# Optimization experiments

Hardware: AMD Instinct MI355X
Metric: run time of the kernel (lower is better)

Reference implementation:

```python
import jax, jax.numpy as jnp
import numpy as np

B, N, D, H = 8, 2048, 128, 4
DH = D // H
EPS_LN = 1e-5


def setup_inputs() -> dict:
    key = jax.random.key(0)
    ks = jax.random.split(key, 9)
    x = jax.random.normal(ks[0], (B, N, D), dtype=jnp.float32)
    u = jax.random.uniform(ks[1], (N, N), dtype=jnp.float32)
    adj = jnp.where(u > 0.5, u, 0.0)
    adj = adj.at[jnp.arange(N), jnp.arange(N)].set(1.0)
    W = jax.random.normal(ks[2], (D, D), dtype=jnp.float32) * (1.0 / np.sqrt(D))
    a_src = jax.random.normal(ks[3], (H, DH), dtype=jnp.float32) * 0.02
    a_dst = jax.random.normal(ks[4], (H, DH), dtype=jnp.float32) * 0.02
    Wo = jax.random.normal(ks[5], (D, D), dtype=jnp.float32) * (1.0 / np.sqrt(D))
    bo = jnp.zeros((D,), dtype=jnp.float32)
    gamma = jnp.ones((D,), dtype=jnp.float32)
    beta = jnp.zeros((D,), dtype=jnp.float32)
    return {"x": x, "adj_static": adj, "W": W, "a_src": a_src, "a_dst": a_dst,
            "Wo": Wo, "bo": bo, "gamma": gamma, "beta": beta}


def reference(x, adj_static, W, a_src, a_dst, Wo, bo, gamma, beta):
    # h: (B, H, N, DH)
    h = (x @ W.T).reshape(B, N, H, DH).transpose(0, 2, 1, 3)
    src = jnp.einsum('bhnd,hd->bhn', h, a_src)  # (B, H, N)
    dst = jnp.einsum('bhnd,hd->bhn', h, a_dst)  # (B, H, N)
    e = jax.nn.leaky_relu(src[..., :, None] + dst[..., None, :], 0.2)  # (B,H,N,N)
    logA = jnp.log(jnp.clip(adj_static, 1e-8))[None, None]
    mask = (adj_static > 0)[None, None]
    e = jnp.where(mask, e + logA, -jnp.inf)
    attn = jax.nn.softmax(e, axis=-1)  # dropout is identity in eval mode
    out = attn @ h  # (B, H, N, DH)
    out = out.transpose(0, 2, 1, 3).reshape(B, N, D)
    out = out @ Wo.T + bo
    y = x + out
    mu = jnp.mean(y, axis=-1, keepdims=True)
    var = jnp.mean(jnp.square(y - mu), axis=-1, keepdims=True)
    return (y - mu) * jax.lax.rsqrt(var + EPS_LN) * gamma + beta
```

## Files before the change

kernel.cpp:

```cpp
#include <hip/hip_runtime.h>

typedef short bf16x8 __attribute__((ext_vector_type(8)));
typedef _Float16 f16x8 __attribute__((ext_vector_type(8)));
typedef float f32x4  __attribute__((ext_vector_type(4)));
typedef float f32x2  __attribute__((ext_vector_type(2)));
typedef int   i32x4  __attribute__((ext_vector_type(4)));
typedef unsigned int u32x2 __attribute__((ext_vector_type(2)));

#define DEV static __device__ __forceinline__
#define LOG2E 1.4426950408889634f

DEV float bfu_to_f(unsigned short s) { return __builtin_bit_cast(float, (unsigned int)s << 16); }
DEV unsigned short f_to_bf(float f) {
  unsigned int u = __builtin_bit_cast(unsigned int, f);
  u += 0x7fffu + ((u >> 16) & 1u);
  return (unsigned short)(u >> 16);
}
DEV unsigned int pack_bf_rne(float lo, float hi) {
  return (unsigned int)f_to_bf(lo) | ((unsigned int)f_to_bf(hi) << 16);
}
DEV unsigned int pk_f16(float a, float b) {
  auto h = __builtin_amdgcn_cvt_pkrtz(a, b);
  return __builtin_bit_cast(unsigned int, h);
}
DEV unsigned short f_to_f16(float a) { return __builtin_bit_cast(unsigned short, (_Float16)a); }
DEV float nexp2(float x) {
#if __has_builtin(__builtin_amdgcn_exp2f)
  return __builtin_amdgcn_exp2f(x);
#else
  return exp2f(x);
#endif
}

DEV bool detect_f32(const void* adj) { return ((const float*)adj)[0] == 1.0f; }

template<bool F32> DEV float ldS(const void* p, size_t i) {
  if constexpr (F32) return ((const float*)p)[i];
  else               return bfu_to_f(((const unsigned short*)p)[i]);
}
template<bool F32> DEV void ld8f(const void* p, size_t i, float* o) {
  if constexpr (F32) {
    const float* f = (const float*)p + i;
    f32x4 a = *(const f32x4*)f, b = *(const f32x4*)(f + 4);
    o[0]=a[0]; o[1]=a[1]; o[2]=a[2]; o[3]=a[3];
    o[4]=b[0]; o[5]=b[1]; o[6]=b[2]; o[7]=b[3];
  } else {
    i32x4 w = *(const i32x4*)((const unsigned short*)p + i);
#pragma unroll
    for (int k = 0; k < 4; ++k) {
      unsigned int u = (unsigned int)w[k];
      o[2*k]   = __builtin_bit_cast(float, u << 16);
      o[2*k+1] = __builtin_bit_cast(float, u & 0xffff0000u);
    }
  }
}
template<bool F32> DEV bf16x8 ldfrag(const void* p, size_t i) {
  if constexpr (F32) {
    float o[8]; ld8f<true>(p, i, o);
    union { bf16x8 v; unsigned short u[8]; } r;
#pragma unroll
    for (int k = 0; k < 8; ++k) r.u[k] = f_to_bf(o[k]);
    return r.v;
  } else {
    return __builtin_bit_cast(bf16x8, *(const i32x4*)((const unsigned short*)p + i));
  }
}


__global__ __launch_bounds__(256) void k_prep(const void* __restrict__ adj,
                                              unsigned short* __restrict__ adjS) {
  const int tid = threadIdx.x, lane = tid & 63, w = tid >> 6;
  const int T = blockIdx.x * 4 + w;
  const int it = T >> 6, jt = T & 63;
  const int m = lane & 15, q = lane >> 4;
  const size_t src = (size_t)(it * 16 + m) * 2048 + jt * 32 + q * 8;
  float f[8];
  if (detect_f32(adj)) ld8f<true>(adj, src, f);
  else                 ld8f<false>(adj, src, f);
  i32x4 o;
#pragma unroll
  for (int k = 0; k < 4; ++k) o[k] = (int)pk_f16(f[2*k], f[2*k+1]);
  *(i32x4*)(adjS + (size_t)T * 512 + lane * 8) = o;
}

template<bool F32> DEV void k_h_body(const void* __restrict__ x, const void* __restrict__ W,
                                     unsigned short* __restrict__ vtS,
                                     unsigned short (&t_s)[16][136]) {
  const int tid = threadIdx.x, lane = tid & 63, wave = tid >> 6;
  const int nt = blockIdx.x >> 3, ct = blockIdx.x & 7;
  const int m = lane & 15, q = lane >> 4;
  bf16x8 wf[4];
#pragma unroll
  for (int k = 0; k < 4; ++k)
    wf[k] = ldfrag<F32>(W, (size_t)(ct * 16 + m) * 128 + q * 8 + k * 32);
#pragma unroll
  for (int s = 0; s < 2; ++s) {
    const int nsub = wave * 2 + s;
    const size_t xr = (size_t)(nt * 128 + nsub * 16 + m) * 128 + q * 8;
    f32x4 acc = {0.f, 0.f, 0.f, 0.f};
#pragma unroll
    for (int k = 0; k < 4; ++k)
      acc = __builtin_amdgcn_mfma_f32_16x16x32_bf16(ldfrag<F32>(x, xr + k * 32), wf[k],
                                                    acc, 0, 0, 0);
    u32x2 w2; w2[0] = pack_bf_rne(acc[0], acc[1]); w2[1] = pack_bf_rne(acc[2], acc[3]);
    *(u32x2*)&t_s[m][nsub * 16 + q * 4] = w2;
  }
  __syncthreads();
  const int row = tid >> 4, c8 = tid & 15;
  const int chg = ct * 16 + row, hh = chg >> 5, dloc = chg & 31;
  const int ng = nt * 128 + c8 * 8, b = ng >> 11, nl = ng & 2047;
  i32x4 v = *(const i32x4*)&t_s[row][c8 * 8];
  float f[8];
#pragma unroll
  for (int k = 0; k < 4; ++k) {
    unsigned int u = (unsigned int)v[k];
    f[2*k]   = __builtin_bit_cast(float, u << 16);
    f[2*k+1] = __builtin_bit_cast(float, u & 0xffff0000u);
  }
  i32x4 o;
#pragma unroll
  for (int k = 0; k < 4; ++k) o[k] = (int)pk_f16(f[2*k], f[2*k+1]);
  const int bh_ = b * 4 + hh;
  const size_t idx = ((size_t)(bh_ * 2 + (dloc >> 4)) * 64 + (nl >> 5)) * 512
                   + (((nl >> 3) & 3) * 16 + (dloc & 15)) * 8;
  *(i32x4*)(vtS + idx) = o;
}
__global__ __launch_bounds__(256) void k_h(const void* x, const void* W,
                                           unsigned short* vtS, const void* adj) {
  __shared__ __align__(16) unsigned short t_s[16][136];
  if (detect_f32(adj)) k_h_body<true>(x, W, vtS, t_s); else k_h_body<false>(x, W, vtS, t_s);
}

template<bool F32> DEV void k_sd_body(const unsigned short* __restrict__ vtS,
                                      const void* __restrict__ a_src, const void* __restrict__ a_dst,
                                      unsigned int* __restrict__ rvh,
                                      unsigned short* __restrict__ Fh,
                                      unsigned short* __restrict__ Hh) {
  const int t = blockIdx.x * 256 + threadIdx.x;
  const int n = t & 2047, bh = t >> 11, hh = bh & 3;
  const unsigned short* colp = vtS + ((size_t)(bh * 2) * 64 + (n >> 5)) * 512
                             + ((n >> 3) & 3) * 128 + (n & 7);
  float s = 0.f, d = 0.f;
#pragma unroll
  for (int dd = 0; dd < 32; ++dd) {
    const float v = (float)__builtin_bit_cast(_Float16,
                      colp[(dd >> 4) * 32768 + (dd & 15) * 8]);
    s += v * ldS<F32>(a_src, hh * 32 + dd);
    d += v * ldS<F32>(a_dst, hh * 32 + dd);
  }
  const float R = nexp2(-0.8f * LOG2E * s);
  const float F = nexp2(LOG2E * d);
  const float H = nexp2(0.2f * LOG2E * d);
  rvh[t] = pk_f16(R, R);
  Fh[t] = f_to_f16(F);
  Hh[t] = f_to_f16(H);
}
__global__ __launch_bounds__(256) void k_sd(const unsigned short* vtS, const void* a_src,
                                            const void* a_dst, unsigned int* rvh,
                                            unsigned short* Fh, unsigned short* Hh,
                                            const void* adj) {
  if (detect_f32(adj)) k_sd_body<true>(vtS, a_src, a_dst, rvh, Fh, Hh);
  else                 k_sd_body<false>(vtS, a_src, a_dst, rvh, Fh, Hh);
}

__global__ __launch_bounds__(256, 4) void k_attn(const unsigned short* __restrict__ adjS,
                                                 const unsigned short* __restrict__ vtS,
                                                 const unsigned int* __restrict__ rvh,
                                                 const unsigned short* __restrict__ Fh,
                                                 const unsigned short* __restrict__ Hh,
                                                 unsigned short* __restrict__ ao) {
  __shared__ __align__(16) float red[3072];
  const int tid = threadIdx.x, lane = tid & 63, wave = tid >> 6;
  const int bh = blockIdx.x & 31, iblk = blockIdx.x >> 5;
  const int b = bh >> 2, hh = bh & 3;
  const int m = lane & 15, q = lane >> 4;
  const int i0 = iblk * 32;
  const int jq0 = wave * 16;

  const unsigned short* ap0 = adjS + ((size_t)(iblk * 2    ) * 64 + jq0) * 512 + lane * 8;
  const unsigned short* ap1 = adjS + ((size_t)(iblk * 2 + 1) * 64 + jq0) * 512 + lane * 8;
  const unsigned short* vp0 = vtS + ((size_t)(bh * 2    ) * 64 + jq0) * 512 + lane * 8;
  const unsigned short* vp1 = vtS + ((size_t)(bh * 2 + 1) * 64 + jq0) * 512 + lane * 8;
  const unsigned short* fpF = Fh + (size_t)bh * 2048 + jq0 * 32 + q * 8;
  const unsigned short* fpH = Hh + (size_t)bh * 2048 + jq0 * 32 + q * 8;

  const unsigned int r0 = rvh[bh * 2048 + i0 + m];
  const unsigned int r1 = rvh[bh * 2048 + i0 + 16 + m];
  const i32x4 rb0 = {(int)r0, (int)r0, (int)r0, (int)r0};
  const i32x4 rb1 = {(int)r1, (int)r1, (int)r1, (int)r1};
  const f16x8 R80 = __builtin_bit_cast(f16x8, rb0);
  const f16x8 R81 = __builtin_bit_cast(f16x8, rb1);
  const i32x4 onev = {0x3C003C00, 0x3C003C00, 0x3C003C00, 0x3C003C00};
  const f16x8 ONE8 = __builtin_bit_cast(f16x8, onev);

  f32x4 accA[2], accB[2], accD[2];
#pragma unroll
  for (int it = 0; it < 2; ++it) {
    accA[it] = f32x4{0.f,0.f,0.f,0.f};
    accB[it] = f32x4{0.f,0.f,0.f,0.f};
    accD[it] = f32x4{0.f,0.f,0.f,0.f};
  }

#pragma unroll
  for (int j = 0; j < 16; ++j) {
    const i32x4 a0 = *(const i32x4*)(ap0 + j * 512);
    const i32x4 a1 = *(const i32x4*)(ap1 + j * 512);
    const i32x4 v0 = *(const i32x4*)(vp0 + j * 512);
    const i32x4 v1 = *(const i32x4*)(vp1 + j * 512);
    const i32x4 ff = *(const i32x4*)(fpF + j * 32);
    const i32x4 fh = *(const i32x4*)(fpH + j * 32);
    const f16x8 F8 = __builtin_bit_cast(f16x8, ff);
    const f16x8 H8 = __builtin_bit_cast(f16x8, fh);
    const f16x8 A0 = __builtin_bit_cast(f16x8, v0);
    const f16x8 A1 = __builtin_bit_cast(f16x8, v1);
    const f16x8 w0 = __builtin_elementwise_max(F8, R80 * H8);
    const f16x8 p0 = __builtin_bit_cast(f16x8, a0) * w0;
    accA[0] = __builtin_amdgcn_mfma_f32_16x16x32_f16(A0,   p0, accA[0], 0, 0, 0);
    accB[0] = __builtin_amdgcn_mfma_f32_16x16x32_f16(A1,   p0, accB[0], 0, 0, 0);
    accD[0] = __builtin_amdgcn_mfma_f32_16x16x32_f16(ONE8, p0, accD[0], 0, 0, 0);
    const f16x8 w1 = __builtin_elementwise_max(F8, R81 * H8);
    const f16x8 p1 = __builtin_bit_cast(f16x8, a1) * w1;
    accA[1] = __builtin_amdgcn_mfma_f32_16x16x32_f16(A0,   p1, accA[1], 0, 0, 0);
    accB[1] = __builtin_amdgcn_mfma_f32_16x16x32_f16(A1,   p1, accB[1], 0, 0, 0);
    accD[1] = __builtin_amdgcn_mfma_f32_16x16x32_f16(ONE8, p1, accD[1], 0, 0, 0);
  }

  if (wave == 1 || wave == 3) {
    const int reg = (wave >> 1) * 1536;
#pragma unroll
    for (int it = 0; it < 2; ++it) {
      const int base = reg + (it * 64 + lane) * 12;
      *(f32x4*)&red[base]     = accA[it];
      *(f32x4*)&red[base + 4] = accB[it];
      red[base + 8] = accD[it][0];
    }
  }
  __syncthreads();
  if (wave == 0 || wave == 2) {
    const int reg = (wave >> 1) * 1536;
#pragma unroll
    for (int it = 0; it < 2; ++it) {
      const int base = reg + (it * 64 + lane) * 12;
      accA[it] += *(const f32x4*)&red[base];
      accB[it] += *(const f32x4*)&red[base + 4];
      accD[it][0] += red[base + 8];
    }
  }
  __syncthreads();
  if (wave == 2) {
#pragma unroll
    for (int it = 0; it < 2; ++it) {
      const int base = (it * 64 + lane) * 12;
      *(f32x4*)&red[base]     = accA[it];
      *(f32x4*)&red[base + 4] = accB[it];
      red[base + 8] = accD[it][0];
    }
  }
  __syncthreads();
  if (wave == 0) {
#pragma unroll
    for (int it = 0; it < 2; ++it) {
      const int base = (it * 64 + lane) * 12;
      const f32x4 a0 = accA[it] + *(const f32x4*)&red[base];
      const f32x4 a1 = accB[it] + *(const f32x4*)&red[base + 4];
      const float den = accD[it][0] + red[base + 8];
      const float inv = 1.f / fmaxf(den, 1e-20f);
      const int il = it * 16 + m;
      unsigned short* op = ao + ((size_t)(b * 2048) + i0 + il) * 128 + hh * 32 + q * 4;
      u32x2 w0, w1;
      w0[0] = pack_bf_rne(a0[0] * inv, a0[1] * inv);
      w0[1] = pack_bf_rne(a0[2] * inv, a0[3] * inv);
      w1[0] = pack_bf_rne(a1[0] * inv, a1[1] * inv);
      w1[1] = pack_bf_rne(a1[2] * inv, a1[3] * inv);
      *(u32x2*)op        = w0;
      *(u32x2*)(op + 16) = w1;
    }
  }
}

template<bool F32> DEV void k_out_body(const unsigned short* __restrict__ ao,
                                       const void* __restrict__ Wo, const void* __restrict__ bo,
                                       const void* __restrict__ x, const void* __restrict__ gamma,
                                       const void* __restrict__ beta, void* __restrict__ out,
                                       float (&y_s)[16][132]) {
  const int tid = threadIdx.x, lane = tid & 63, wave = tid >> 6;
  const int m = lane & 15, q = lane >> 4;
  const int rbase = blockIdx.x * 16;
  bf16x8 af[4];
#pragma unroll
  for (int k = 0; k < 4; ++k)
    af[k] = ldfrag<false>(ao, ((size_t)(rbase + m)) * 128 + q * 8 + k * 32);
  f32x4 acc[2] = {{0.f,0.f,0.f,0.f},{0.f,0.f,0.f,0.f}};
#pragma unroll
  for (int ct = 0; ct < 2; ++ct) {
    const size_t wrow = (size_t)(wave * 32 + ct * 16 + m) * 128 + q * 8;
#pragma unroll
    for (int k = 0; k < 4; ++k)
      acc[ct] = __builtin_amdgcn_mfma_f32_16x16x32_bf16(af[k], ldfrag<F32>(Wo, wrow + k * 32),
                                                        acc[ct], 0, 0, 0);
  }
#pragma unroll
  for (int ct = 0; ct < 2; ++ct) {
    const int c = wave * 32 + ct * 16 + m;
    const float bov = ldS<F32>(bo, c);
#pragma unroll
    for (int r = 0; r < 4; ++r) {
      const int row = q * 4 + r;
      y_s[row][c] = acc[ct][r] + bov + ldS<F32>(x, (size_t)(rbase + row) * 128 + c);
    }
  }
  __syncthreads();
  const int r = tid >> 4, c16 = tid & 15;
  float vals[8], sum = 0.f, sq = 0.f;
#pragma unroll
  for (int k = 0; k < 8; ++k) {
    const float v = y_s[r][c16 * 8 + k];
    vals[k] = v; sum += v; sq += v * v;
  }
#pragma unroll
  for (int msk = 1; msk < 16; msk <<= 1) {
    sum += __shfl_xor(sum, msk, 16);
    sq  += __shfl_xor(sq,  msk, 16);
  }
  const float mu  = sum * (1.f / 128.f);
  const float var = fmaxf(sq * (1.f / 128.f) - mu * mu, 0.f);
  const float rstd = rsqrtf(var + 1e-5f);
  float o[8];
#pragma unroll
  for (int k = 0; k < 8; ++k) {
    const int c = c16 * 8 + k;
    o[k] = (vals[k] - mu) * rstd * ldS<F32>(gamma, c) + ldS<F32>(beta, c);
  }
  const size_t obase = (size_t)(rbase + r) * 128 + c16 * 8;
  if constexpr (F32) {
    float* op = (float*)out + obase;
    f32x4 w0 = {o[0],o[1],o[2],o[3]}, w1 = {o[4],o[5],o[6],o[7]};
    *(f32x4*)op = w0; *(f32x4*)(op + 4) = w1;
  } else {
    union { unsigned short u[8]; i32x4 v; } ob;
#pragma unroll
    for (int k = 0; k < 8; ++k) ob.u[k] = f_to_bf(o[k]);
    *(i32x4*)((unsigned short*)out + obase) = ob.v;
  }
}
__global__ __launch_bounds__(256) void k_out(const unsigned short* ao, const void* Wo,
                                             const void* bo, const void* x, const void* gamma,
                                             const void* beta, void* out, const void* adj) {
  __shared__ __align__(16) float y_s[16][132];
  if (detect_f32(adj)) k_out_body<true>(ao, Wo, bo, x, gamma, beta, out, y_s);
  else                 k_out_body<false>(ao, Wo, bo, x, gamma, beta, out, y_s);
}

extern "C" void kernel_launch(void* const* d_in, const int* in_sizes, int n_in,
                              void* d_out, int out_size, void* d_ws, size_t ws_size,
                              hipStream_t stream) {
  const void* x     = d_in[0];
  const void* adj   = d_in[1];
  const void* W     = d_in[2];
  const void* a_src = d_in[3];
  const void* a_dst = d_in[4];
  const void* Wo    = d_in[5];
  const void* bo    = d_in[6];
  const void* gamma = d_in[7];
  const void* beta  = d_in[8];

  char* ws = (char*)d_ws;
  unsigned short* adjS  = (unsigned short*)ws;
  unsigned short* vtS   = (unsigned short*)(ws + 8388608);
  unsigned short* ao_ws = (unsigned short*)(ws + 12582912);
  unsigned int*   rvh   = (unsigned int*)(ws + 16777216);
  unsigned short* Fh    = (unsigned short*)(ws + 17039360);
  unsigned short* Hh    = (unsigned short*)(ws + 17170432);

  k_prep<<<2048, 256, 0, stream>>>(adj, adjS);
  k_h   <<<1024, 256, 0, stream>>>(x, W, vtS, adj);
  k_sd  <<<256,  256, 0, stream>>>(vtS, a_src, a_dst, rvh, Fh, Hh, adj);
  k_attn<<<2048, 256, 0, stream>>>(adjS, vtS, rvh, Fh, Hh, ao_ws);
  k_out <<<1024, 256, 0, stream>>>(ao_ws, Wo, bo, x, gamma, beta, d_out, adj);
}
```

Baseline: 145.4 us.

## Double attention row tile per block and swizzle block order for cache reuse

```diff
diff --git a/kernel.cpp b/kernel.cpp
--- a/kernel.cpp
+++ b/kernel.cpp
@@ -169,42 +169,41 @@
                                                  const unsigned short* __restrict__ Fh,
                                                  const unsigned short* __restrict__ Hh,
                                                  unsigned short* __restrict__ ao) {
-  __shared__ __align__(16) float red[3072];
+  __shared__ __align__(16) float red[6144];
   const int tid = threadIdx.x, lane = tid & 63, wave = tid >> 6;
-  const int bh = blockIdx.x & 31, iblk = blockIdx.x >> 5;
+  const int swz = (blockIdx.x & 7) * 128 + (blockIdx.x >> 3);
+  const int bh = swz & 31, iblk = swz >> 5;
   const int b = bh >> 2, hh = bh & 3;
   const int m = lane & 15, q = lane >> 4;
-  const int i0 = iblk * 32;
+  const int i0 = iblk * 64;
   const int jq0 = wave * 16;
 
-  const unsigned short* ap0 = adjS + ((size_t)(iblk * 2    ) * 64 + jq0) * 512 + lane * 8;
-  const unsigned short* ap1 = adjS + ((size_t)(iblk * 2 + 1) * 64 + jq0) * 512 + lane * 8;
+  const unsigned short* ap  = adjS + ((size_t)(iblk * 4) * 64 + jq0) * 512 + lane * 8;
   const unsigned short* vp0 = vtS + ((size_t)(bh * 2    ) * 64 + jq0) * 512 + lane * 8;
   const unsigned short* vp1 = vtS + ((size_t)(bh * 2 + 1) * 64 + jq0) * 512 + lane * 8;
   const unsigned short* fpF = Fh + (size_t)bh * 2048 + jq0 * 32 + q * 8;
   const unsigned short* fpH = Hh + (size_t)bh * 2048 + jq0 * 32 + q * 8;
 
-  const unsigned int r0 = rvh[bh * 2048 + i0 + m];
-  const unsigned int r1 = rvh[bh * 2048 + i0 + 16 + m];
-  const i32x4 rb0 = {(int)r0, (int)r0, (int)r0, (int)r0};
-  const i32x4 rb1 = {(int)r1, (int)r1, (int)r1, (int)r1};
-  const f16x8 R80 = __builtin_bit_cast(f16x8, rb0);
-  const f16x8 R81 = __builtin_bit_cast(f16x8, rb1);
+  f16x8 R8[4];
+#pragma unroll
+  for (int it = 0; it < 4; ++it) {
+    const unsigned int r = rvh[bh * 2048 + i0 + it * 16 + m];
+    const i32x4 rb = {(int)r, (int)r, (int)r, (int)r};
+    R8[it] = __builtin_bit_cast(f16x8, rb);
+  }
   const i32x4 onev = {0x3C003C00, 0x3C003C00, 0x3C003C00, 0x3C003C00};
   const f16x8 ONE8 = __builtin_bit_cast(f16x8, onev);
 
-  f32x4 accA[2], accB[2], accD[2];
-#pragma unroll
-  for (int it = 0; it < 2; ++it) {
+  f32x4 accA[4], accB[4], accD[4];
+#pragma unroll
+  for (int it = 0; it < 4; ++it) {
     accA[it] = f32x4{0.f,0.f,0.f,0.f};
     accB[it] = f32x4{0.f,0.f,0.f,0.f};
     accD[it] = f32x4{0.f,0.f,0.f,0.f};
   }
 
-#pragma unroll
+#pragma unroll 4
   for (int j = 0; j < 16; ++j) {
-    const i32x4 a0 = *(const i32x4*)(ap0 + j * 512);
-    const i32x4 a1 = *(const i32x4*)(ap1 + j * 512);
     const i32x4 v0 = *(const i32x4*)(vp0 + j * 512);
     const i32x4 v1 = *(const i32x4*)(vp1 + j * 512);
     const i32x4 ff = *(const i32x4*)(fpF + j * 32);
@@ -213,22 +212,21 @@
     const f16x8 H8 = __builtin_bit_cast(f16x8, fh);
     const f16x8 A0 = __builtin_bit_cast(f16x8, v0);
     const f16x8 A1 = __builtin_bit_cast(f16x8, v1);
-    const f16x8 w0 = __builtin_elementwise_max(F8, R80 * H8);
-    const f16x8 p0 = __builtin_bit_cast(f16x8, a0) * w0;
-    accA[0] = __builtin_amdgcn_mfma_f32_16x16x32_f16(A0,   p0, accA[0], 0, 0, 0);
-    accB[0] = __builtin_amdgcn_mfma_f32_16x16x32_f16(A1,   p0, accB[0], 0, 0, 0);
-    accD[0] = __builtin_amdgcn_mfma_f32_16x16x32_f16(ONE8, p0, accD[0], 0, 0, 0);
-    const f16x8 w1 = __builtin_elementwise_max(F8, R81 * H8);
-    const f16x8 p1 = __builtin_bit_cast(f16x8, a1) * w1;
-    accA[1] = __builtin_amdgcn_mfma_f32_16x16x32_f16(A0,   p1, accA[1], 0, 0, 0);
-    accB[1] = __builtin_amdgcn_mfma_f32_16x16x32_f16(A1,   p1, accB[1], 0, 0, 0);
-    accD[1] = __builtin_amdgcn_mfma_f32_16x16x32_f16(ONE8, p1, accD[1], 0, 0, 0);
+#pragma unroll
+    for (int it = 0; it < 4; ++it) {
+      const i32x4 av = *(const i32x4*)(ap + it * 32768 + j * 512);
+      const f16x8 w8 = __builtin_elementwise_max(F8, R8[it] * H8);
+      const f16x8 p8 = __builtin_bit_cast(f16x8, av) * w8;
+      accA[it] = __builtin_amdgcn_mfma_f32_16x16x32_f16(A0,   p8, accA[it], 0, 0, 0);
+      accB[it] = __builtin_amdgcn_mfma_f32_16x16x32_f16(A1,   p8, accB[it], 0, 0, 0);
+      accD[it] = __builtin_amdgcn_mfma_f32_16x16x32_f16(ONE8, p8, accD[it], 0, 0, 0);
+    }
   }
 
   if (wave == 1 || wave == 3) {
-    const int reg = (wave >> 1) * 1536;
-#pragma unroll
-    for (int it = 0; it < 2; ++it) {
+    const int reg = (wave >> 1) * 3072;
+#pragma unroll
+    for (int it = 0; it < 4; ++it) {
       const int base = reg + (it * 64 + lane) * 12;
       *(f32x4*)&red[base]     = accA[it];
       *(f32x4*)&red[base + 4] = accB[it];
@@ -237,9 +235,9 @@
   }
   __syncthreads();
   if (wave == 0 || wave == 2) {
-    const int reg = (wave >> 1) * 1536;
-#pragma unroll
-    for (int it = 0; it < 2; ++it) {
+    const int reg = (wave >> 1) * 3072;
+#pragma unroll
+    for (int it = 0; it < 4; ++it) {
       const int base = reg + (it * 64 + lane) * 12;
       accA[it] += *(const f32x4*)&red[base];
       accB[it] += *(const f32x4*)&red[base + 4];
@@ -249,7 +247,7 @@
   __syncthreads();
   if (wave == 2) {
 #pragma unroll
-    for (int it = 0; it < 2; ++it) {
+    for (int it = 0; it < 4; ++it) {
       const int base = (it * 64 + lane) * 12;
       *(f32x4*)&red[base]     = accA[it];
       *(f32x4*)&red[base + 4] = accB[it];
@@ -259,7 +257,7 @@
   __syncthreads();
   if (wave == 0) {
 #pragma unroll
-    for (int it = 0; it < 2; ++it) {
+    for (int it = 0; it < 4; ++it) {
       const int base = (it * 64 + lane) * 12;
       const f32x4 a0 = accA[it] + *(const f32x4*)&red[base];
       const f32x4 a1 = accB[it] + *(const f32x4*)&red[base + 4];
@@ -375,6 +373,6 @@
   k_prep<<<2048, 256, 0, stream>>>(adj, adjS);
   k_h   <<<1024, 256, 0, stream>>>(x, W, vtS, adj);
   k_sd  <<<256,  256, 0, stream>>>(vtS, a_src, a_dst, rvh, Fh, Hh, adj);
-  k_attn<<<2048, 256, 0, stream>>>(adjS, vtS, rvh, Fh, Hh, ao_ws);
+  k_attn<<<1024, 256, 0, stream>>>(adjS, vtS, rvh, Fh, Hh, ao_ws);
   k_out <<<1024, 256, 0, stream>>>(ao_ws, Wo, bo, x, gamma, beta, d_out, adj);
 }
```

Result: slower. 175.9 us (+21.0%).

## Merge prep and projection kernels; double-buffer attention loads with MFMA priority

Applied to the files above, without the earlier changes.

```diff
diff --git a/kernel.cpp b/kernel.cpp
--- a/kernel.cpp
+++ b/kernel.cpp
@@ -67,27 +67,25 @@
 }
 
 
-__global__ __launch_bounds__(256) void k_prep(const void* __restrict__ adj,
-                                              unsigned short* __restrict__ adjS) {
+template<bool F32> DEV void prep_part(const void* __restrict__ adj,
+                                      unsigned short* __restrict__ adjS, int blk) {
   const int tid = threadIdx.x, lane = tid & 63, w = tid >> 6;
-  const int T = blockIdx.x * 4 + w;
+  const int T = blk * 4 + w;
   const int it = T >> 6, jt = T & 63;
   const int m = lane & 15, q = lane >> 4;
   const size_t src = (size_t)(it * 16 + m) * 2048 + jt * 32 + q * 8;
   float f[8];
-  if (detect_f32(adj)) ld8f<true>(adj, src, f);
-  else                 ld8f<false>(adj, src, f);
+  ld8f<F32>(adj, src, f);
   i32x4 o;
 #pragma unroll
   for (int k = 0; k < 4; ++k) o[k] = (int)pk_f16(f[2*k], f[2*k+1]);
   *(i32x4*)(adjS + (size_t)T * 512 + lane * 8) = o;
 }
-
-template<bool F32> DEV void k_h_body(const void* __restrict__ x, const void* __restrict__ W,
-                                     unsigned short* __restrict__ vtS,
-                                     unsigned short (&t_s)[16][136]) {
+template<bool F32> DEV void h_part(const void* __restrict__ x, const void* __restrict__ W,
+                                   unsigned short* __restrict__ vtS,
+                                   unsigned short (&t_s)[16][136], int blk) {
   const int tid = threadIdx.x, lane = tid & 63, wave = tid >> 6;
-  const int nt = blockIdx.x >> 3, ct = blockIdx.x & 7;
+  const int nt = blk >> 3, ct = blk & 7;
   const int m = lane & 15, q = lane >> 4;
   bf16x8 wf[4];
 #pragma unroll
@@ -125,10 +123,17 @@
                    + (((nl >> 3) & 3) * 16 + (dloc & 15)) * 8;
   *(i32x4*)(vtS + idx) = o;
 }
-__global__ __launch_bounds__(256) void k_h(const void* x, const void* W,
-                                           unsigned short* vtS, const void* adj) {
+__global__ __launch_bounds__(256) void k_pre(const void* adj, const void* x, const void* W,
+                                             unsigned short* adjS, unsigned short* vtS) {
   __shared__ __align__(16) unsigned short t_s[16][136];
-  if (detect_f32(adj)) k_h_body<true>(x, W, vtS, t_s); else k_h_body<false>(x, W, vtS, t_s);
+  const bool f32 = detect_f32(adj);
+  if (blockIdx.x < 2048) {
+    if (f32) prep_part<true>(adj, adjS, blockIdx.x);
+    else     prep_part<false>(adj, adjS, blockIdx.x);
+  } else {
+    if (f32) h_part<true>(x, W, vtS, t_s, blockIdx.x - 2048);
+    else     h_part<false>(x, W, vtS, t_s, blockIdx.x - 2048);
+  }
 }
 
 template<bool F32> DEV void k_sd_body(const unsigned short* __restrict__ vtS,
@@ -161,6 +166,45 @@
                                             const void* adj) {
   if (detect_f32(adj)) k_sd_body<true>(vtS, a_src, a_dst, rvh, Fh, Hh);
   else                 k_sd_body<false>(vtS, a_src, a_dst, rvh, Fh, Hh);
+}
+
+struct Pref {
+  i32x4 a0, a1;
+  i32x4 v0, v1;
+  i32x4 ff, fh;
+};
+
+DEV void pload(Pref& p, const unsigned short* ap0, const unsigned short* ap1,
+               const unsigned short* vp0, const unsigned short* vp1,
+               const unsigned short* fpF, const unsigned short* fpH, int j) {
+  p.a0 = *(const i32x4*)(ap0 + j * 512);
+  p.a1 = *(const i32x4*)(ap1 + j * 512);
+  p.v0 = *(const i32x4*)(vp0 + j * 512);
+  p.v1 = *(const i32x4*)(vp1 + j * 512);
+  p.ff = *(const i32x4*)(fpF + j * 32);
+  p.fh = *(const i32x4*)(fpH + j * 32);
+}
+
+DEV void pcompute(const Pref& p, const f16x8 R80, const f16x8 R81, const f16x8 ONE8,
+                  f32x4 (&accA)[2], f32x4 (&accB)[2], f32x4 (&accD)[2]) {
+  const f16x8 F8 = __builtin_bit_cast(f16x8, p.ff);
+  const f16x8 H8 = __builtin_bit_cast(f16x8, p.fh);
+  const f16x8 A0 = __builtin_bit_cast(f16x8, p.v0);
+  const f16x8 A1 = __builtin_bit_cast(f16x8, p.v1);
+  const f16x8 w0 = __builtin_elementwise_max(F8, R80 * H8);
+  const f16x8 p0 = __builtin_bit_cast(f16x8, p.a0) * w0;
+  __builtin_amdgcn_s_setprio(1);
+  accA[0] = __builtin_amdgcn_mfma_f32_16x16x32_f16(A0,   p0, accA[0], 0, 0, 0);
+  accB[0] = __builtin_amdgcn_mfma_f32_16x16x32_f16(A1,   p0, accB[0], 0, 0, 0);
+  accD[0] = __builtin_amdgcn_mfma_f32_16x16x32_f16(ONE8, p0, accD[0], 0, 0, 0);
+  __builtin_amdgcn_s_setprio(0);
+  const f16x8 w1 = __builtin_elementwise_max(F8, R81 * H8);
+  const f16x8 p1 = __builtin_bit_cast(f16x8, p.a1) * w1;
+  __builtin_amdgcn_s_setprio(1);
+  accA[1] = __builtin_amdgcn_mfma_f32_16x16x32_f16(A0,   p1, accA[1], 0, 0, 0);
+  accB[1] = __builtin_amdgcn_mfma_f32_16x16x32_f16(A1,   p1, accB[1], 0, 0, 0);
+  accD[1] = __builtin_amdgcn_mfma_f32_16x16x32_f16(ONE8, p1, accD[1], 0, 0, 0);
+  __builtin_amdgcn_s_setprio(0);
 }
 
 __global__ __launch_bounds__(256, 4) void k_attn(const unsigned short* __restrict__ adjS,
@@ -201,28 +245,14 @@
     accD[it] = f32x4{0.f,0.f,0.f,0.f};
   }
 
-#pragma unroll
-  for (int j = 0; j < 16; ++j) {
-    const i32x4 a0 = *(const i32x4*)(ap0 + j * 512);
-    const i32x4 a1 = *(const i32x4*)(ap1 + j * 512);
-    const i32x4 v0 = *(const i32x4*)(vp0 + j * 512);
-    const i32x4 v1 = *(const i32x4*)(vp1 + j * 512);
-    const i32x4 ff = *(const i32x4*)(fpF + j * 32);
-    const i32x4 fh = *(const i32x4*)(fpH + j * 32);
-    const f16x8 F8 = __builtin_bit_cast(f16x8, ff);
-    const f16x8 H8 = __builtin_bit_cast(f16x8, fh);
-    const f16x8 A0 = __builtin_bit_cast(f16x8, v0);
-    const f16x8 A1 = __builtin_bit_cast(f16x8, v1);
-    const f16x8 w0 = __builtin_elementwise_max(F8, R80 * H8);
-    const f16x8 p0 = __builtin_bit_cast(f16x8, a0) * w0;
-    accA[0] = __builtin_amdgcn_mfma_f32_16x16x32_f16(A0,   p0, accA[0], 0, 0, 0);
-    accB[0] = __builtin_amdgcn_mfma_f32_16x16x32_f16(A1,   p0, accB[0], 0, 0, 0);
-    accD[0] = __builtin_amdgcn_mfma_f32_16x16x32_f16(ONE8, p0, accD[0], 0, 0, 0);
-    const f16x8 w1 = __builtin_elementwise_max(F8, R81 * H8);
-    const f16x8 p1 = __builtin_bit_cast(f16x8, a1) * w1;
-    accA[1] = __builtin_amdgcn_mfma_f32_16x16x32_f16(A0,   p1, accA[1], 0, 0, 0);
-    accB[1] = __builtin_amdgcn_mfma_f32_16x16x32_f16(A1,   p1, accB[1], 0, 0, 0);
-    accD[1] = __builtin_amdgcn_mfma_f32_16x16x32_f16(ONE8, p1, accD[1], 0, 0, 0);
+  Pref pA, pB;
+  pload(pA, ap0, ap1, vp0, vp1, fpF, fpH, 0);
+#pragma unroll
+  for (int c = 0; c < 16; c += 2) {
+    pload(pB, ap0, ap1, vp0, vp1, fpF, fpH, c + 1);
+    pcompute(pA, R80, R81, ONE8, accA, accB, accD);
+    if (c + 2 < 16) pload(pA, ap0, ap1, vp0, vp1, fpF, fpH, c + 2);
+    pcompute(pB, R80, R81, ONE8, accA, accB, accD);
   }
 
   if (wave == 1 || wave == 3) {
@@ -372,8 +402,7 @@
   unsigned short* Fh    = (unsigned short*)(ws + 17039360);
   unsigned short* Hh    = (unsigned short*)(ws + 17170432);
 
-  k_prep<<<2048, 256, 0, stream>>>(adj, adjS);
-  k_h   <<<1024, 256, 0, stream>>>(x, W, vtS, adj);
+  k_pre <<<3072, 256, 0, stream>>>(adj, x, W, adjS, vtS);
   k_sd  <<<256,  256, 0, stream>>>(vtS, a_src, a_dst, rvh, Fh, Hh, adj);
   k_attn<<<2048, 256, 0, stream>>>(adjS, vtS, rvh, Fh, Hh, ao_ws);
   k_out <<<1024, 256, 0, stream>>>(ao_ws, Wo, bo, x, gamma, beta, d_out, adj);
```

Result: no change. 147.1 us (+1.2%).
